# Optimization experiments

Measured on AMD Instinct MI355X. Metric: run time of the kernel, lower is better.

The kernel has to match this reference:

```python
import jax, jax.numpy as jnp
import numpy as np

D = 1024
H = 16
DH = D // H  # 64
EPS = 1e-5


def _ln(x, w, b=None):
    mu = jnp.mean(x, axis=-1, keepdims=True)
    var = jnp.var(x, axis=-1, keepdims=True)
    y = (x - mu) * jax.lax.rsqrt(var + EPS) * w
    return y + b if b is not None else y


def _rotate_half(x):
    x1, x2 = jnp.split(x, 2, axis=-1)
    return jnp.concatenate([-x2, x1], axis=-1)


def _rope(q, k):
    # q, k: [B, L, H, DH]; rotary over sequence dim (ESM-style half-split rotation)
    L = q.shape[1]
    inv_freq = 1.0 / (10000.0 ** (jnp.arange(0, DH, 2, dtype=jnp.float32) / DH))
    freqs = jnp.arange(L, dtype=jnp.float32)[:, None] * inv_freq[None, :]  # [L, DH/2]
    emb = jnp.concatenate([freqs, freqs], axis=-1)  # [L, DH]
    cos = jnp.cos(emb)[None, :, None, :]  # [1, L, 1, DH]
    sin = jnp.sin(emb)[None, :, None, :]
    q = q * cos + _rotate_half(q) * sin
    k = k * cos + _rotate_half(k) * sin
    return q, k


def setup_inputs() -> dict:
    key = jax.random.key(0)
    ks = jax.random.split(key, 8)
    B, L = 2, 2048
    x = jax.random.normal(ks[0], (B, L, D), dtype=jnp.float32)
    seq_id = jnp.sort(jax.random.randint(ks[1], (B, L), 0, 8), axis=-1)
    s = 1.0 / np.sqrt(D)
    return {
        "x": x,
        "seq_id": seq_id,
        "ln1_w": jnp.ones((D,), jnp.float32),
        "ln1_b": jnp.zeros((D,), jnp.float32),
        "w_qkv": jax.random.normal(ks[2], (3 * D, D), dtype=jnp.float32) * s,
        "q_ln_w": jnp.ones((D,), jnp.float32),
        "k_ln_w": jnp.ones((D,), jnp.float32),
        "out_w": jax.random.normal(ks[3], (D, D), dtype=jnp.float32) * s,
    }


def reference(x, seq_id, ln1_w, ln1_b, w_qkv, q_ln_w, k_ln_w, out_w):
    B, L, _ = x.shape
    h = _ln(x, ln1_w, ln1_b)
    qkv = jnp.einsum("bld,ed->ble", h, w_qkv)  # [B, L, 3D]
    q, k, v = jnp.split(qkv, 3, axis=-1)
    q = _ln(q, q_ln_w)
    k = _ln(k, k_ln_w)
    q = q.reshape(B, L, H, DH)
    k = k.reshape(B, L, H, DH)
    q, k = _rope(q, k)
    q = q.transpose(0, 2, 1, 3)  # [B, H, L, DH]
    k = k.transpose(0, 2, 1, 3)
    v = v.reshape(B, L, H, DH).transpose(0, 2, 1, 3)
    scale = 1.0 / np.sqrt(DH)
    scores = jnp.einsum("bhld,bhmd->bhlm", q, k) * scale  # [B, H, L, L]
    mask = (seq_id[:, None, :, None] == seq_id[:, None, None, :])  # [B, 1, L, L]
    scores = jnp.where(mask, scores, -jnp.inf)
    attn = jax.nn.softmax(scores, axis=-1)
    ctx = jnp.einsum("bhlm,bhmd->bhld", attn, v)  # [B, H, L, DH]
    ctx = ctx.transpose(0, 2, 1, 3).reshape(B, L, D)
    return jnp.einsum("bld,ed->ble", ctx, out_w)
```

## Files before the change

### kernel.cpp

```cpp
#include <hip/hip_runtime.h>
#include <hip/hip_bf16.h>
#include <math.h>

#define D 1024
#define H 16
#define DH 64
#define L 2048
#define B 2
#define NROW (B * L)
#define EPS 1e-5f

typedef _Float16 half8 __attribute__((ext_vector_type(8)));
typedef _Float16 half4v __attribute__((ext_vector_type(4)));
typedef float f32x4 __attribute__((ext_vector_type(4)));

__global__ __launch_bounds__(256) void prep_kernel(const float* __restrict__ x,
                                                   const float* __restrict__ lw,
                                                   const float* __restrict__ lb,
                                                   _Float16* __restrict__ h16,
                                                   const float* __restrict__ wqkv,
                                                   _Float16* __restrict__ wqkv16,
                                                   const float* __restrict__ outw,
                                                   _Float16* __restrict__ outw16,
                                                   const int* __restrict__ seq_id,
                                                   int* __restrict__ lo,
                                                   int* __restrict__ hi,
                                                   float2* __restrict__ rtab) {
    int blk = blockIdx.x;
    int t = threadIdx.x;
    if (blk < 4096) {
        int r = blk;
        const float* xr = x + (size_t)r * D;
        float4 v = *(const float4*)&xr[t * 4];
        float s = v.x + v.y + v.z + v.w;
        float sq = v.x * v.x + v.y * v.y + v.z * v.z + v.w * v.w;
        for (int off = 32; off > 0; off >>= 1) {
            s += __shfl_xor(s, off, 64);
            sq += __shfl_xor(sq, off, 64);
        }
        __shared__ float ls[4], lq[4];
        int wave = t >> 6;
        if ((t & 63) == 0) { ls[wave] = s; lq[wave] = sq; }
        __syncthreads();
        float S = ls[0] + ls[1] + ls[2] + ls[3];
        float Q = lq[0] + lq[1] + lq[2] + lq[3];
        float mu = S / (float)D;
        float rs = rsqrtf(Q / (float)D - mu * mu + EPS);
        float4 w4 = *(const float4*)&lw[t * 4];
        float4 b4 = *(const float4*)&lb[t * 4];
        half4v o = {(_Float16)((v.x - mu) * rs * w4.x + b4.x),
                    (_Float16)((v.y - mu) * rs * w4.y + b4.y),
                    (_Float16)((v.z - mu) * rs * w4.z + b4.z),
                    (_Float16)((v.w - mu) * rs * w4.w + b4.w)};
        *(half4v*)&h16[(size_t)r * D + t * 4] = o;
    } else if (blk < 6144) {
        int base = blk - 4096;
        const float* src;
        _Float16* dst;
        if (base < 1536) { src = wqkv; dst = wqkv16; }
        else             { src = outw; dst = outw16; base -= 1536; }
        int i = (base * 256 + t) * 8;
        float4 a = *(const float4*)&src[i];
        float4 b = *(const float4*)&src[i + 4];
        half8 h = {(_Float16)a.x, (_Float16)a.y, (_Float16)a.z, (_Float16)a.w,
                   (_Float16)b.x, (_Float16)b.y, (_Float16)b.z, (_Float16)b.w};
        *(half8*)&dst[i] = h;
    } else if (blk < 6160) {
        int idx = (blk - 6144) * 256 + t;
        int b = idx / L, l = idx - b * L;
        const int* row = seq_id + (size_t)b * L;
        int v = row[l];
        int a = 0, c = L;
        while (a < c) { int m = (a + c) >> 1; if (row[m] < v) a = m + 1; else c = m; }
        lo[idx] = a;
        a = 0; c = L;
        while (a < c) { int m = (a + c) >> 1; if (row[m] <= v) a = m + 1; else c = m; }
        hi[idx] = a;
    } else {
        int idx = (blk - 6160) * 256 + t;
        int l = idx >> 5, fi = idx & 31;
        float invf = expf(-(float)fi * 0.28782313662425572f);
        float sn, cs;
        sincosf((float)l * invf, &sn, &cs);
        rtab[idx] = make_float2(cs, sn);
    }
}

template <typename OutT, int BM, int BN>
__global__ __launch_bounds__(256) void gemm_f16_kernel(const _Float16* __restrict__ A,
                                                       const _Float16* __restrict__ W,
                                                       OutT* __restrict__ C, int N) {
    constexpr int WM = BM / 2, WN = BN / 2;
    constexpr int MT = WM / 16, NT = WN / 16;
    __shared__ _Float16 As[2][BM * 32];
    __shared__ _Float16 Bs[2][BN * 32];
    int t = threadIdx.x;
    int w = t >> 6, lane = t & 63;
    int quad = lane >> 4, col = lane & 15;
    int m0 = blockIdx.y * BM, n0 = blockIdx.x * BN;
    int mw = (w >> 1) * WM, nw = (w & 1) * WN;
    int sw = (col >> 1) & 3;

    f32x4 acc[MT][NT] = {};

    auto stage = [&](int k0, int buf) {
#pragma unroll
        for (int i = 0; i < BM / 64; i++) {
            int e = t + i * 256;
            int row = e >> 2, kc = (e & 3) ^ ((row >> 1) & 3);
            __builtin_amdgcn_global_load_lds(
                (const __attribute__((address_space(1))) void*)&A[(size_t)(m0 + row) * 1024 + k0 + kc * 8],
                (__attribute__((address_space(3))) void*)&As[buf][e * 8], 16, 0, 0);
        }
#pragma unroll
        for (int i = 0; i < BN / 64; i++) {
            int e = t + i * 256;
            int row = e >> 2, kc = (e & 3) ^ ((row >> 1) & 3);
            __builtin_amdgcn_global_load_lds(
                (const __attribute__((address_space(1))) void*)&W[(size_t)(n0 + row) * 1024 + k0 + kc * 8],
                (__attribute__((address_space(3))) void*)&Bs[buf][e * 8], 16, 0, 0);
        }
    };

    stage(0, 0);
    int cur = 0;
    for (int k0 = 0; k0 < 1024; k0 += 32) {
        __syncthreads();
        if (k0 + 32 < 1024) stage(k0 + 32, cur ^ 1);
        half8 af[MT], bf[NT];
#pragma unroll
        for (int mt = 0; mt < MT; mt++)
            af[mt] = *(const half8*)&As[cur][(mw + mt * 16 + col) * 32 + ((quad ^ sw) << 3)];
#pragma unroll
        for (int nt = 0; nt < NT; nt++)
            bf[nt] = *(const half8*)&Bs[cur][(nw + nt * 16 + col) * 32 + ((quad ^ sw) << 3)];
#pragma unroll
        for (int mt = 0; mt < MT; mt++)
#pragma unroll
            for (int nt = 0; nt < NT; nt++)
                acc[mt][nt] = __builtin_amdgcn_mfma_f32_16x16x32_f16(af[mt], bf[nt], acc[mt][nt], 0, 0, 0);
        cur ^= 1;
    }

#pragma unroll
    for (int mt = 0; mt < MT; mt++)
#pragma unroll
        for (int nt = 0; nt < NT; nt++)
#pragma unroll
            for (int r = 0; r < 4; r++) {
                int row = m0 + mw + mt * 16 + quad * 4 + r;
                int cc = n0 + nw + nt * 16 + col;
                C[(size_t)row * N + cc] = (OutT)acc[mt][nt][r];
            }
}

__global__ __launch_bounds__(256) void mid_kernel(const _Float16* __restrict__ qkv,
                                                  const float* __restrict__ qw,
                                                  const float* __restrict__ kw,
                                                  const float2* __restrict__ rtab,
                                                  _Float16* __restrict__ q_r,
                                                  _Float16* __restrict__ k_r,
                                                  _Float16* __restrict__ v_t) {
    __shared__ float ls[4], lq[4];
    __shared__ _Float16 T[64][64];
    int blk = blockIdx.x;
    int t = threadIdx.x;
    if (blk < 8192) {
        int r = blk >> 1;
        int which = blk & 1;
        const _Float16* src = qkv + (size_t)r * 3072 + which * 1024;
        const float* w = which ? kw : qw;
        _Float16* dst = which ? k_r : q_r;

        float vals[4];
        float s = 0.f, sq = 0.f;
#pragma unroll
        for (int i = 0; i < 4; i++) {
            float v = (float)src[t + i * 256];
            vals[i] = v;
            s += v;
            sq += v * v;
        }
        for (int off = 32; off > 0; off >>= 1) {
            s += __shfl_xor(s, off, 64);
            sq += __shfl_xor(sq, off, 64);
        }
        int wave = t >> 6;
        if ((t & 63) == 0) { ls[wave] = s; lq[wave] = sq; }
        __syncthreads();
        float S = ls[0] + ls[1] + ls[2] + ls[3];
        float Q = lq[0] + lq[1] + lq[2] + lq[3];
        float mu = S / 1024.f;
        float rs = rsqrtf(Q / 1024.f - mu * mu + EPS);

        int l = r & (L - 1);
        int b = r >> 11;
#pragma unroll
        for (int i = 0; i < 4; i++) {
            int j = t + i * 256;
            float y = (vals[i] - mu) * rs * w[j];
            float p = __shfl_xor(y, 32, 64);
            int dh = j & 63, hh = j >> 6;
            float2 cs = rtab[l * 32 + (dh & 31)];
            float out = (dh < 32) ? (y * cs.x - p * cs.y) : (y * cs.x + p * cs.y);
            dst[((size_t)((b * H + hh) * L + l)) * 64 + dh] = (_Float16)out;
        }
    } else {
        int vb = blk - 8192;
        int bh = vb >> 5;
        int b = bh >> 4, h = bh & 15;
        int l0 = (vb & 31) * 64;
#pragma unroll
        for (int i = 0; i < 2; i++) {
            int e = t + i * 256;
            int li = e >> 3, ch = e & 7;
            half8 hv = *(const half8*)&qkv[((size_t)(b * L + l0 + li)) * 3072 + 2048 + h * 64 + ch * 8];
            *(half8*)&T[li][((ch ^ (li >> 3)) & 7) * 8] = hv;
        }
        __syncthreads();
#pragma unroll
        for (int i = 0; i < 2; i++) {
            int e = t + i * 256;
            int d = e >> 3, ch = e & 7;
            half8 hv;
#pragma unroll
            for (int j = 0; j < 8; j++)
                hv[j] = T[ch * 8 + j][((((d >> 3) ^ ch) & 7) * 8) + (d & 7)];
            *(half8*)&v_t[((size_t)(bh * 64 + d)) * 2048 + l0 + ch * 8] = hv;
        }
    }
}

__global__ __launch_bounds__(256) void attn_mfma_kernel(const _Float16* __restrict__ q_r,
                                                        const _Float16* __restrict__ k_r,
                                                        const _Float16* __restrict__ v_t,
                                                        const int* __restrict__ lo_arr,
                                                        const int* __restrict__ hi_arr,
                                                        _Float16* __restrict__ ctx) {
    __shared__ _Float16 Ks[2][64][64];
    __shared__ _Float16 Vs[2][64][64];
    __shared__ _Float16 Ps[4][16][64];
    int bh = blockIdx.y;
    int b = bh >> 4, h = bh & 15;
    int l0 = blockIdx.x * 64;
    int t = threadIdx.x;
    int w = t >> 6, lane = t & 63;
    int quad = lane >> 4, col = lane & 15;
    int rbase = l0 + w * 16;

    int blo = lo_arr[b * L + l0] & ~63;
    int bhi = hi_arr[b * L + l0 + 63];

    auto stage = [&](int m0, int buf) {
#pragma unroll
        for (int i = 0; i < 2; i++) {
            int e = t + i * 256;
            int row = e >> 3, ch = e & 7;
            int sch = ch ^ (row & 7);
            __builtin_amdgcn_global_load_lds(
                (const __attribute__((address_space(1))) void*)&k_r[((size_t)(bh * L + m0 + row)) * 64 + sch * 8],
                (__attribute__((address_space(3))) void*)&Ks[buf][row][ch * 8], 16, 0, 0);
            __builtin_amdgcn_global_load_lds(
                (const __attribute__((address_space(1))) void*)&v_t[((size_t)(bh * 64 + row)) * 2048 + m0 + sch * 8],
                (__attribute__((address_space(3))) void*)&Vs[buf][row][ch * 8], 16, 0, 0);
        }
    };

    stage(blo, 0);

    half8 qf0, qf1;
    {
        const _Float16* qp = q_r + ((size_t)(bh * L + rbase + col)) * 64 + quad * 8;
        qf0 = *(const half8*)qp;
        qf1 = *(const half8*)(qp + 32);
    }
    int lo_c = lo_arr[b * L + rbase + col];
    int hi_c = hi_arr[b * L + rbase + col];
    int wlo = __shfl(lo_c, 15, 64);
    int whi = __shfl(hi_c, 0, 64);

    f32x4 o[4] = {};
    float m_run = -1e30f, l_run = 0.f;
    const float SCL = 0.125f * 1.4426950408889634f;
    int swz = (col & 7) << 3;
    int src = (lane & 48) | ((lane & 48) >> 2);

    int cur = 0;
    for (int m0 = blo; m0 < bhi; m0 += 64) {
        __syncthreads();
        if (m0 + 64 < bhi) stage(m0 + 64, cur ^ 1);

        f32x4 s[4] = {};
#pragma unroll
        for (int nt = 0; nt < 4; nt++) {
            int key = nt * 16 + col;
            const _Float16* kp = &Ks[cur][key][0];
            half8 kf0 = *(const half8*)&kp[(quad ^ (key & 7)) * 8];
            half8 kf1 = *(const half8*)&kp[((quad + 4) ^ (key & 7)) * 8];
            s[nt] = __builtin_amdgcn_mfma_f32_16x16x32_f16(kf0, qf0, s[nt], 0, 0, 0);
            s[nt] = __builtin_amdgcn_mfma_f32_16x16x32_f16(kf1, qf1, s[nt], 0, 0, 0);
        }

        float p[4][4];
        bool full = (m0 >= wlo) && (m0 + 64 <= whi);
        if (full) {
#pragma unroll
            for (int nt = 0; nt < 4; nt++)
#pragma unroll
                for (int r = 0; r < 4; r++) p[nt][r] = s[nt][r] * SCL;
        } else {
#pragma unroll
            for (int nt = 0; nt < 4; nt++) {
                int kb = m0 + nt * 16 + quad * 4;
#pragma unroll
                for (int r = 0; r < 4; r++) {
                    int key = kb + r;
                    p[nt][r] = (key >= lo_c && key < hi_c) ? s[nt][r] * SCL : -INFINITY;
                }
            }
        }

        float tmax = p[0][0];
#pragma unroll
        for (int nt = 0; nt < 4; nt++)
#pragma unroll
            for (int r = 0; r < 4; r++) tmax = fmaxf(tmax, p[nt][r]);
        tmax = fmaxf(tmax, __shfl_xor(tmax, 16, 64));
        tmax = fmaxf(tmax, __shfl_xor(tmax, 32, 64));
        float nm = fmaxf(m_run, tmax);
        float corr = exp2f(m_run - nm);
        m_run = nm;
        float rs = 0.f;
#pragma unroll
        for (int nt = 0; nt < 4; nt++)
#pragma unroll
            for (int r = 0; r < 4; r++) {
                float e2 = exp2f(p[nt][r] - nm);
                p[nt][r] = e2;
                rs += e2;
            }
        rs += __shfl_xor(rs, 16, 64);
        rs += __shfl_xor(rs, 32, 64);
        l_run = l_run * corr + rs;

#pragma unroll
        for (int nt = 0; nt < 4; nt++) {
            half4v pk = {(_Float16)p[nt][0], (_Float16)p[nt][1],
                         (_Float16)p[nt][2], (_Float16)p[nt][3]};
            *(half4v*)&Ps[w][col][(nt * 16 + quad * 4) ^ swz] = pk;
        }

#pragma unroll
        for (int r = 0; r < 4; r++) {
            float c4 = __shfl(corr, src + r, 64);
            o[0][r] *= c4; o[1][r] *= c4; o[2][r] *= c4; o[3][r] *= c4;
        }

        half8 pf0 = *(const half8*)&Ps[w][col][(quad * 8) ^ swz];
        half8 pf1 = *(const half8*)&Ps[w][col][(32 + quad * 8) ^ swz];
#pragma unroll
        for (int nt = 0; nt < 4; nt++) {
            int dr = nt * 16 + col;
            const _Float16* vp = &Vs[cur][dr][0];
            half8 vf0 = *(const half8*)&vp[(quad ^ (dr & 7)) * 8];
            half8 vf1 = *(const half8*)&vp[((quad + 4) ^ (dr & 7)) * 8];
            o[nt] = __builtin_amdgcn_mfma_f32_16x16x32_f16(pf0, vf0, o[nt], 0, 0, 0);
            o[nt] = __builtin_amdgcn_mfma_f32_16x16x32_f16(pf1, vf1, o[nt], 0, 0, 0);
        }
        cur ^= 1;
    }

#pragma unroll
    for (int r = 0; r < 4; r++) {
        float linv = 1.f / __shfl(l_run, src + r, 64);
        int row = rbase + quad * 4 + r;
#pragma unroll
        for (int nt = 0; nt < 4; nt++)
            ctx[((size_t)(b * L + row)) * 1024 + h * 64 + nt * 16 + col] =
                (_Float16)(o[nt][r] * linv);
    }
}

extern "C" void kernel_launch(void* const* d_in, const int* in_sizes, int n_in,
                              void* d_out, int out_size, void* d_ws, size_t ws_size,
                              hipStream_t stream) {
    const float* x      = (const float*)d_in[0];
    const int*   seq_id = (const int*)d_in[1];
    const float* ln1_w  = (const float*)d_in[2];
    const float* ln1_b  = (const float*)d_in[3];
    const float* w_qkv  = (const float*)d_in[4];
    const float* q_ln_w = (const float*)d_in[5];
    const float* k_ln_w = (const float*)d_in[6];
    const float* out_w  = (const float*)d_in[7];
    float* out = (float*)d_out;

    char* ws = (char*)d_ws;
    int*      lo     = (int*)(ws);
    int*      hi     = (int*)(ws + (64 << 10));
    float2*   rtab   = (float2*)(ws + (128 << 10));
    _Float16* h16    = (_Float16*)(ws + (1ull << 20));
    _Float16* wqkv16 = (_Float16*)(ws + (10ull << 20));
    _Float16* outw16 = (_Float16*)(ws + (17ull << 20));
    _Float16* qkv16  = (_Float16*)(ws + (20ull << 20));
    _Float16* q_r    = (_Float16*)(ws + (45ull << 20));
    _Float16* k_r    = (_Float16*)(ws + (54ull << 20));
    _Float16* v_t    = (_Float16*)(ws + (63ull << 20));
    _Float16* ctx16  = (_Float16*)(ws + (72ull << 20));

    prep_kernel<<<dim3(6416), dim3(256), 0, stream>>>(
        x, ln1_w, ln1_b, h16, w_qkv, wqkv16, out_w, outw16, seq_id, lo, hi, rtab);
    gemm_f16_kernel<_Float16, 128, 128><<<dim3(3072 / 128, NROW / 128), dim3(256), 0, stream>>>(
        h16, wqkv16, qkv16, 3072);
    mid_kernel<<<dim3(9216), dim3(256), 0, stream>>>(qkv16, q_ln_w, k_ln_w, rtab, q_r, k_r, v_t);
    attn_mfma_kernel<<<dim3(L / 64, B * H), dim3(256), 0, stream>>>(q_r, k_r, v_t, lo, hi, ctx16);
    gemm_f16_kernel<float, 128, 64><<<dim3(1024 / 64, NROW / 128), dim3(256), 0, stream>>>(
        ctx16, outw16, out, 1024);

    (void)in_sizes; (void)n_in; (void)out_size; (void)ws_size;
}
```

Measured before the change: 190.2 us.

## Add 256x256 eight-wave pipelined QKV GEMM and XCD-aware tile remapping

```diff
diff --git a/kernel.cpp b/kernel.cpp
--- a/kernel.cpp
+++ b/kernel.cpp
@@ -86,6 +86,118 @@
     }
 }
 
+#define LDA_HALF(BUF, MH, DST)                                                      \
+    _Pragma("unroll") for (int mt = 0; mt < 4; mt++) {                              \
+        int row_ = mw + (MH) * 64 + mt * 16 + col;                                  \
+        _Pragma("unroll") for (int kk = 0; kk < 2; kk++)                            \
+            DST[mt][kk] = *(const half8*)&As[BUF][row_][((kk * 4 + quad) ^ (row_ & 7)) * 8]; \
+    }
+
+#define LDB_HALF(BUF, NH, DST)                                                      \
+    _Pragma("unroll") for (int nt = 0; nt < 2; nt++) {                              \
+        int row_ = nw + (NH) * 32 + nt * 16 + col;                                  \
+        _Pragma("unroll") for (int kk = 0; kk < 2; kk++)                            \
+            DST[nt][kk] = *(const half8*)&Bs[BUF][row_][((kk * 4 + quad) ^ (row_ & 7)) * 8]; \
+    }
+
+#define MMA_QUAD(MH, NH, AF, BF)                                                    \
+    __builtin_amdgcn_s_setprio(1);                                                  \
+    _Pragma("unroll") for (int mt = 0; mt < 4; mt++)                                \
+    _Pragma("unroll") for (int nt = 0; nt < 2; nt++) {                              \
+        acc[(MH) * 4 + mt][(NH) * 2 + nt] = __builtin_amdgcn_mfma_f32_16x16x32_f16( \
+            AF[mt][0], BF[nt][0], acc[(MH) * 4 + mt][(NH) * 2 + nt], 0, 0, 0);      \
+        acc[(MH) * 4 + mt][(NH) * 2 + nt] = __builtin_amdgcn_mfma_f32_16x16x32_f16( \
+            AF[mt][1], BF[nt][1], acc[(MH) * 4 + mt][(NH) * 2 + nt], 0, 0, 0);      \
+    }                                                                               \
+    __builtin_amdgcn_s_setprio(0);
+
+__global__ __launch_bounds__(512, 2) void gemm1_8phase(const _Float16* __restrict__ A,
+                                                       const _Float16* __restrict__ W,
+                                                       _Float16* __restrict__ C) {
+    __shared__ _Float16 As[2][256][64];
+    __shared__ _Float16 Bs[2][256][64];
+    int t = threadIdx.x;
+    int w = t >> 6, lane = t & 63;
+    int quad = lane >> 4, col = lane & 15;
+
+    int i = blockIdx.y * 12 + blockIdx.x;
+    int xcd = i & 7, j = i >> 3;
+    int tm = (xcd >> 1) * 4 + j / 6;
+    int tn = (xcd & 1) * 6 + j % 6;
+    int m0 = tm * 256, n0 = tn * 256;
+    int mw = (w >> 2) * 128, nw = (w & 3) * 64;
+
+    f32x4 acc[8][4] = {};
+
+    auto stageA = [&](int kt, int buf, int half) {
+#pragma unroll
+        for (int ii = 0; ii < 2; ii++) {
+            int e = half * 1024 + ii * 512 + t;
+            int row = e >> 3, ch = e & 7;
+            int sch = ch ^ (row & 7);
+            __builtin_amdgcn_global_load_lds(
+                (const __attribute__((address_space(1))) void*)&A[(size_t)(m0 + row) * 1024 + kt * 64 + sch * 8],
+                (__attribute__((address_space(3))) void*)&As[buf][row][ch * 8], 16, 0, 0);
+        }
+    };
+    auto stageB = [&](int kt, int buf, int half) {
+#pragma unroll
+        for (int ii = 0; ii < 2; ii++) {
+            int e = half * 1024 + ii * 512 + t;
+            int row = e >> 3, ch = e & 7;
+            int sch = ch ^ (row & 7);
+            __builtin_amdgcn_global_load_lds(
+                (const __attribute__((address_space(1))) void*)&W[(size_t)(n0 + row) * 1024 + kt * 64 + sch * 8],
+                (__attribute__((address_space(3))) void*)&Bs[buf][row][ch * 8], 16, 0, 0);
+        }
+    };
+
+    stageA(0, 0, 0); stageA(0, 0, 1); stageB(0, 0, 0); stageB(0, 0, 1);
+    asm volatile("s_waitcnt vmcnt(0)" ::: "memory");
+    __builtin_amdgcn_s_barrier();
+
+    half8 af[4][2], bf0[2][2], bf1[2][2];
+    for (int kt = 0; kt < 16; kt++) {
+        int buf = kt & 1, nbuf = buf ^ 1;
+        bool more = (kt + 1) < 16;
+
+        LDA_HALF(buf, 0, af);
+        LDB_HALF(buf, 0, bf0);
+        if (more) stageA(kt + 1, nbuf, 0);
+        __builtin_amdgcn_s_barrier();
+        MMA_QUAD(0, 0, af, bf0);
+        __builtin_amdgcn_s_barrier();
+
+        LDB_HALF(buf, 1, bf1);
+        if (more) stageA(kt + 1, nbuf, 1);
+        __builtin_amdgcn_s_barrier();
+        MMA_QUAD(0, 1, af, bf1);
+        __builtin_amdgcn_s_barrier();
+
+        LDA_HALF(buf, 1, af);
+        if (more) stageB(kt + 1, nbuf, 0);
+        __builtin_amdgcn_s_barrier();
+        MMA_QUAD(1, 1, af, bf1);
+        __builtin_amdgcn_s_barrier();
+
+        if (more) stageB(kt + 1, nbuf, 1);
+        MMA_QUAD(1, 0, af, bf0);
+        asm volatile("s_waitcnt vmcnt(0)" ::: "memory");
+        __builtin_amdgcn_s_barrier();
+    }
+
+#pragma unroll
+    for (int mt = 0; mt < 8; mt++)
+#pragma unroll
+        for (int nt = 0; nt < 4; nt++)
+#pragma unroll
+            for (int r = 0; r < 4; r++) {
+                int row = m0 + mw + mt * 16 + quad * 4 + r;
+                int cc = n0 + nw + nt * 16 + col;
+                C[(size_t)row * 3072 + cc] = (_Float16)acc[mt][nt][r];
+            }
+}
+
 template <typename OutT, int BM, int BN>
 __global__ __launch_bounds__(256) void gemm_f16_kernel(const _Float16* __restrict__ A,
                                                        const _Float16* __restrict__ W,
@@ -97,7 +209,11 @@
     int t = threadIdx.x;
     int w = t >> 6, lane = t & 63;
     int quad = lane >> 4, col = lane & 15;
-    int m0 = blockIdx.y * BM, n0 = blockIdx.x * BN;
+    int nx = gridDim.x;
+    int ib = blockIdx.y * nx + blockIdx.x;
+    int nwg = nx * gridDim.y;
+    int ni = (ib & 7) * (nwg >> 3) + (ib >> 3);
+    int m0 = (ni / nx) * BM, n0 = (ni % nx) * BN;
     int mw = (w >> 1) * WM, nw = (w & 1) * WN;
     int sw = (col >> 1) & 3;
 
@@ -409,8 +525,7 @@
 
     prep_kernel<<<dim3(6416), dim3(256), 0, stream>>>(
         x, ln1_w, ln1_b, h16, w_qkv, wqkv16, out_w, outw16, seq_id, lo, hi, rtab);
-    gemm_f16_kernel<_Float16, 128, 128><<<dim3(3072 / 128, NROW / 128), dim3(256), 0, stream>>>(
-        h16, wqkv16, qkv16, 3072);
+    gemm1_8phase<<<dim3(12, 16), dim3(512), 0, stream>>>(h16, wqkv16, qkv16);
     mid_kernel<<<dim3(9216), dim3(256), 0, stream>>>(qkv16, q_ln_w, k_ln_w, rtab, q_r, k_r, v_t);
     attn_mfma_kernel<<<dim3(L / 64, B * H), dim3(256), 0, stream>>>(q_r, k_r, v_t, lo, hi, ctx16);
     gemm_f16_kernel<float, 128, 64><<<dim3(1024 / 64, NROW / 128), dim3(256), 0, stream>>>(
```

Result: no change. 190.9 us (+0.4%).
